# Performance work log

Hardware: AMD Instinct MI355X
Metric: run time of the kernel (lower is better)

Reference implementation:

```python
import jax, jax.numpy as jnp
import numpy as np

B, S, E, H = 2, 2048, 1024, 16
D = E // H  # head_dim = 64

def setup_inputs() -> dict:
    key = jax.random.key(0)
    k1, k2, k3 = jax.random.split(key, 3)
    x = jax.random.normal(k1, (B, S, E), dtype=jnp.float32)
    W_attn = jax.random.normal(k2, (E, 3 * E), dtype=jnp.float32) * 0.02
    b_attn = jnp.zeros((3 * E,), dtype=jnp.float32)
    W_proj = jax.random.normal(k3, (E, E), dtype=jnp.float32) * 0.02
    b_proj = jnp.zeros((E,), dtype=jnp.float32)
    return {"x": x, "W_attn": W_attn, "b_attn": b_attn, "W_proj": W_proj, "b_proj": b_proj}

def reference(x, W_attn, b_attn, W_proj, b_proj):
    bsz, seq, emb = x.shape
    # fused QKV projection (Conv1D == linear with [in,out] weight)
    qkv = x @ W_attn + b_attn                       # [B,S,3E]
    q, k, v = jnp.split(qkv, 3, axis=-1)
    def to_heads(t):
        return t.reshape(bsz, seq, H, D).transpose(0, 2, 1, 3)  # [B,H,S,D]
    q, k, v = to_heads(q), to_heads(k), to_heads(v)
    scale = jnp.float32(D) ** -0.5
    scores = jnp.einsum('bhqd,bhkd->bhqk', q, k) * scale        # [B,H,S,S]
    causal = jnp.tril(jnp.ones((seq, seq), dtype=bool))
    scores = jnp.where(causal, scores, jnp.float32(-jnp.inf))
    attn = jax.nn.softmax(scores, axis=-1)
    out = jnp.einsum('bhqk,bhkd->bhqd', attn, v)                # [B,H,S,D]
    out = out.transpose(0, 2, 1, 3).reshape(bsz, seq, emb)
    y = out @ W_proj + b_proj
    return y
```

## Files before the change

kernel.cpp:

```cpp
#include <hip/hip_runtime.h>
#include <hip/hip_bf16.h>


typedef __bf16 bf16;
typedef __bf16 bf16x4 __attribute__((ext_vector_type(4)));
typedef __bf16 bf16x8 __attribute__((ext_vector_type(8)));
typedef float  f32x4  __attribute__((ext_vector_type(4)));

#define MNEG (-1.0e30f)
#define QSCALE 0.1803368801f

__device__ __forceinline__ void gload16(const bf16* g, bf16* l) {
  __builtin_amdgcn_global_load_lds((const __attribute__((address_space(1))) void*)g,
                                   (__attribute__((address_space(3))) void*)l, 16, 0, 0);
}

__global__ __launch_bounds__(256) void prep_k(const float* __restrict__ x, bf16* __restrict__ xb,
                                              const float* __restrict__ Wa, bf16* __restrict__ WaT,
                                              const float* __restrict__ Wp, bf16* __restrict__ WpT) {
  const int bid = blockIdx.x;
  if (bid < 2048) {
    const int i = bid * 256 + threadIdx.x;
    f32x4 a = ((const f32x4*)x)[2 * i], b = ((const f32x4*)x)[2 * i + 1];
    bf16x8 o;
    for (int j = 0; j < 4; ++j) { o[j] = (bf16)a[j]; o[4 + j] = (bf16)b[j]; }
    ((bf16x8*)xb)[i] = o;
    return;
  }
  __shared__ bf16 t[64][68];
  const float* in; bf16* out; int C, cx, cy;
  if (bid < 2816) { in = Wa; out = WaT; C = 3072; const int tt = bid - 2048; cx = tt % 48; cy = tt / 48; }
  else            { in = Wp; out = WpT; C = 1024; const int tt = bid - 2816; cx = tt % 16; cy = tt / 16; }
  const int R = 1024;
  const int c0 = cx * 64, r0 = cy * 64;
  const int lr = threadIdx.x >> 4;
  const int lc = (threadIdx.x & 15) * 4;
  for (int i = 0; i < 4; ++i) {
    int r = lr + i * 16;
    f32x4 v = *(const f32x4*)(in + (size_t)(r0 + r) * C + c0 + lc);
    bf16x4 b;
    for (int j = 0; j < 4; ++j) b[j] = (bf16)v[j];
    *(bf16x4*)&t[r][lc] = b;
  }
  __syncthreads();
  for (int i = 0; i < 4; ++i) {
    int c = lr + i * 16;
    bf16x4 v;
    for (int j = 0; j < 4; ++j) v[j] = t[lc + j][c];
    *(bf16x4*)(out + (size_t)(c0 + c) * R + r0 + lc) = v;
  }
}

template <int MODE, int BN>
__global__ __launch_bounds__(256) void gemm_bt(const bf16* __restrict__ A,
                                               const bf16* __restrict__ Bt,
                                               const float* __restrict__ bias,
                                               float* __restrict__ C,
                                               bf16* __restrict__ Qo,
                                               bf16* __restrict__ Ko,
                                               bf16* __restrict__ Vo,
                                               int M, int N, int K) {
  constexpr int NT = BN / 32;
  __shared__ bf16 As0[128 * 32], As1[128 * 32];
  __shared__ bf16 Bs0[BN * 32],  Bs1[BN * 32];
  const int tid = threadIdx.x;
  const int w = tid >> 6, l = tid & 63;
  const int nx = gridDim.x;
  const int nwg = nx * gridDim.y;
  const int flat = blockIdx.y * nx + blockIdx.x;
  const int swz = (flat & 7) * (nwg >> 3) + (flat >> 3);
  const int m0 = (swz / nx) * 128, n0 = (swz % nx) * BN;
  const int wm = w >> 1, wn = w & 1;
  const int fr = l & 15, fg = l >> 4;
  const int srow = l >> 2;
  const int scol = (l & 3) * 8;

  f32x4 acc[4][NT] = {};

  for (int k0 = 0; k0 < K; k0 += 64) {
    __syncthreads();
    for (int c = 0; c < 2; ++c) {
      const int rowA = 32 * w + 16 * c + srow;
      gload16(A + (size_t)(m0 + rowA) * K + k0 + scol,      As0 + (32 * w + 16 * c) * 32);
      gload16(A + (size_t)(m0 + rowA) * K + k0 + 32 + scol, As1 + (32 * w + 16 * c) * 32);
    }
    for (int c = 0; c < BN / 64; ++c) {
      const int rb = (BN / 64) * 16 * w + 16 * c;
      gload16(Bt + (size_t)(n0 + rb + srow) * K + k0 + scol,      Bs0 + rb * 32);
      gload16(Bt + (size_t)(n0 + rb + srow) * K + k0 + 32 + scol, Bs1 + rb * 32);
    }
    __syncthreads();

    bf16x8 af[4][2], bfv[NT][2];
    for (int mt = 0; mt < 4; ++mt) {
      af[mt][0] = *(const bf16x8*)(As0 + (wm * 64 + mt * 16 + fr) * 32 + 8 * fg);
      af[mt][1] = *(const bf16x8*)(As1 + (wm * 64 + mt * 16 + fr) * 32 + 8 * fg);
    }
    for (int nt = 0; nt < NT; ++nt) {
      bfv[nt][0] = *(const bf16x8*)(Bs0 + (wn * (BN / 2) + nt * 16 + fr) * 32 + 8 * fg);
      bfv[nt][1] = *(const bf16x8*)(Bs1 + (wn * (BN / 2) + nt * 16 + fr) * 32 + 8 * fg);
    }
    for (int mt = 0; mt < 4; ++mt)
      for (int nt = 0; nt < NT; ++nt) {
        acc[mt][nt] = __builtin_amdgcn_mfma_f32_16x16x32_bf16(af[mt][0], bfv[nt][0], acc[mt][nt], 0, 0, 0);
        acc[mt][nt] = __builtin_amdgcn_mfma_f32_16x16x32_bf16(af[mt][1], bfv[nt][1], acc[mt][nt], 0, 0, 0);
      }
  }

  for (int mt = 0; mt < 4; ++mt) {
    for (int nt = 0; nt < NT; ++nt) {
      const int row0 = m0 + wm * 64 + mt * 16 + 4 * fg;
      const int col = n0 + wn * (BN / 2) + nt * 16 + fr;
      const float bv = bias[col];
      if (MODE == 0) {
        for (int r = 0; r < 4; ++r)
          C[(size_t)(row0 + r) * N + col] = acc[mt][nt][r] + bv;
      } else {
        const int which = col >> 10, h = (col >> 6) & 15, d = col & 63;
        const int b = row0 >> 11, s = row0 & 2047;
        if (which == 2) {
          bf16x4 vv;
          for (int r = 0; r < 4; ++r) vv[r] = (bf16)(acc[mt][nt][r] + bv);
          *(bf16x4*)(Vo + ((size_t)(b * 16 + h) * 64 + d) * 2048 + s) = vv;
        } else if (which == 0) {
          for (int r = 0; r < 4; ++r)
            Qo[((size_t)(b * 16 + h) * 2048 + s + r) * 64 + d] =
                (bf16)((acc[mt][nt][r] + bv) * QSCALE);
        } else {
          for (int r = 0; r < 4; ++r)
            Ko[((size_t)(b * 16 + h) * 2048 + s + r) * 64 + d] = (bf16)(acc[mt][nt][r] + bv);
        }
      }
    }
  }
}

__global__ __launch_bounds__(256, 3) void attn_k(const bf16* __restrict__ Qw,
                                                 const bf16* __restrict__ Kw,
                                                 const bf16* __restrict__ VtG,
                                                 bf16* __restrict__ AO) {
  __shared__ bf16 Ks[128 * 72];
  __shared__ bf16 Vt[64 * 136];
  __shared__ bf16 Ps[4 * 16 * 72];
  const int tid = threadIdx.x, w = tid >> 6, l = tid & 63;
  const int bid = blockIdx.x;
  const int bh = ((bid & 7) << 2) | ((bid >> 3) & 3);
  const int qt = 31 - (bid >> 5);
  const int q0 = qt * 64;
  const int fr = l & 15, fg = l >> 4;
  const size_t base = (size_t)bh * 2048 * 64;
  const int qw0 = q0 + w * 16;
  const int q = qw0 + fr;
  bf16* Pw = Ps + w * 16 * 72;
  const int r8 = tid >> 3, c8 = (tid & 7) * 8;
  const int r16 = tid >> 4, c16 = (tid & 15) * 8;

  bf16x8 qf[2];
  for (int t = 0; t < 2; ++t)
    qf[t] = *(const bf16x8*)(Qw + base + (size_t)(qw0 + fr) * 64 + 32 * t + 8 * fg);

  f32x4 oacc[4] = {};
  float lsum = 0.f;
  bf16x8 kreg[4], vreg[4];

  auto load_tile = [&](int kt) {
    for (int c = 0; c < 4; ++c) {
      kreg[c] = *(const bf16x8*)(Kw + base + (size_t)(kt + r8 + 32 * c) * 64 + c8);
      vreg[c] = *(const bf16x8*)(VtG + base + (size_t)(r16 + 16 * c) * 2048 + kt + c16);
    }
  };
  auto write_tile = [&]() {
    for (int c = 0; c < 4; ++c) {
      *(bf16x8*)(Ks + (r8 + 32 * c) * 72 + c8) = kreg[c];
      *(bf16x8*)(Vt + (r16 + 16 * c) * 136 + c16) = vreg[c];
    }
  };

  load_tile(0);
  write_tile();
  __syncthreads();

  for (int kt = 0; kt <= q0; kt += 128) {
    const bool havenext = (kt + 128 <= q0);
    if (havenext) load_tile(kt + 128);

    for (int h = 0; h < 2; ++h) {
      const int kh = kt + 64 * h;
      if (kh > q0) break;

      f32x4 sc[4];
      __builtin_amdgcn_s_setprio(1);
      for (int c = 0; c < 4; ++c) {
        bf16x8 kf0 = *(const bf16x8*)(Ks + (64 * h + c * 16 + fr) * 72 + 8 * fg);
        bf16x8 kf1 = *(const bf16x8*)(Ks + (64 * h + c * 16 + fr) * 72 + 32 + 8 * fg);
        f32x4 z = {};
        z = __builtin_amdgcn_mfma_f32_16x16x32_bf16(kf0, qf[0], z, 0, 0, 0);
        sc[c] = __builtin_amdgcn_mfma_f32_16x16x32_bf16(kf1, qf[1], z, 0, 0, 0);
      }
      __builtin_amdgcn_s_setprio(0);

      const bool need_mask = (kh + 63 > qw0);
      float psum = 0.f;
      for (int c = 0; c < 4; ++c) {
        bf16x4 pb;
        for (int r = 0; r < 4; ++r) {
          float s = sc[c][r];
          if (need_mask && (kh + c * 16 + 4 * fg + r > q)) s = MNEG;
          const float pv = __builtin_amdgcn_exp2f(s);
          psum += pv;
          pb[r] = (bf16)pv;
        }
        *(bf16x4*)(Pw + fr * 72 + c * 16 + 4 * fg) = pb;
      }
      psum += __shfl_xor(psum, 16, 64);
      psum += __shfl_xor(psum, 32, 64);
      lsum += psum;

      asm volatile("" ::: "memory");
      __builtin_amdgcn_s_setprio(1);
      for (int t = 0; t < 2; ++t) {
        bf16x8 pa = *(const bf16x8*)(Pw + fr * 72 + 32 * t + 8 * fg);
        for (int dt = 0; dt < 4; ++dt) {
          bf16x8 vf = *(const bf16x8*)(Vt + (dt * 16 + fr) * 136 + 64 * h + 32 * t + 8 * fg);
          oacc[dt] = __builtin_amdgcn_mfma_f32_16x16x32_bf16(pa, vf, oacc[dt], 0, 0, 0);
        }
      }
      __builtin_amdgcn_s_setprio(0);
      asm volatile("" ::: "memory");
    }

    if (!havenext) break;
    __syncthreads();
    write_tile();
    __syncthreads();
  }

  const int b = bh >> 4, h = bh & 15;
  float linv[4];
  for (int r = 0; r < 4; ++r)
    linv[r] = 1.f / __shfl(lsum, (l & 48) | (4 * fg + r), 64);
  for (int dt = 0; dt < 4; ++dt)
    for (int r = 0; r < 4; ++r) {
      const int qq = qw0 + 4 * fg + r;
      AO[(size_t)(b * 2048 + qq) * 1024 + h * 64 + dt * 16 + fr] =
          (bf16)(oacc[dt][r] * linv[r]);
    }
}

extern "C" void kernel_launch(void* const* d_in, const int* in_sizes, int n_in,
                              void* d_out, int out_size, void* d_ws, size_t ws_size,
                              hipStream_t stream) {
  const float* x      = (const float*)d_in[0];
  const float* W_attn = (const float*)d_in[1];
  const float* b_attn = (const float*)d_in[2];
  const float* W_proj = (const float*)d_in[3];
  const float* b_proj = (const float*)d_in[4];
  float* out = (float*)d_out;

  char* ws = (char*)d_ws;
  bf16* WaT = (bf16*)(ws);
  bf16* WpT = (bf16*)(ws + 6291456);
  bf16* Qw  = (bf16*)(ws + 8388608);
  bf16* Kw  = (bf16*)(ws + 16777216);
  bf16* VtG = (bf16*)(ws + 25165824);
  bf16* AO  = (bf16*)(ws + 33554432);
  bf16* xb  = AO;

  prep_k<<<3072, 256, 0, stream>>>(x, xb, W_attn, WaT, W_proj, WpT);

  gemm_bt<1, 128><<<dim3(24, 32), 256, 0, stream>>>(
      xb, WaT, b_attn, nullptr, Qw, Kw, VtG, 4096, 3072, 1024);

  attn_k<<<1024, 256, 0, stream>>>(Qw, Kw, VtG, AO);

  gemm_bt<0, 64><<<dim3(16, 32), 256, 0, stream>>>(
      AO, WpT, b_proj, out, nullptr, nullptr, nullptr, 4096, 1024, 1024);
}
```

Baseline: 109.5 us.

## Split heavy causal attention tiles over KV range and merge in normalization kernel

The heaviest query tiles (the upper half of the sequence) are split into two blocks, each covering half of the KV range. Each writes unnormalized fp32 partial outputs and row sums to workspace. A new norm_k kernel adds the two partials, divides by the combined sum and writes bf16 output. This balances work across the grid and shortens the critical-path block, at the cost of an extra launch plus fp32 partial traffic. It works without a running max because scores are bounded and use a fixed offset. The split path runs only when the workspace is large enough.

```diff
diff --git a/kernel.cpp b/kernel.cpp
--- a/kernel.cpp
+++ b/kernel.cpp
@@ -135,18 +135,43 @@
   }
 }
 
+template <int SPLIT>
 __global__ __launch_bounds__(256, 3) void attn_k(const bf16* __restrict__ Qw,
                                                  const bf16* __restrict__ Kw,
                                                  const bf16* __restrict__ VtG,
-                                                 bf16* __restrict__ AO) {
+                                                 bf16* __restrict__ AO,
+                                                 float* __restrict__ Op,
+                                                 float* __restrict__ Lp) {
   __shared__ bf16 Ks[128 * 72];
   __shared__ bf16 Vt[64 * 136];
   __shared__ bf16 Ps[4 * 16 * 72];
   const int tid = threadIdx.x, w = tid >> 6, l = tid & 63;
   const int bid = blockIdx.x;
-  const int bh = ((bid & 7) << 2) | ((bid >> 3) & 3);
-  const int qt = 31 - (bid >> 5);
+
+  int bh, qt, part; bool heavy;
+  if (SPLIT && bid < 1024) {
+    bh = ((bid & 7) << 2) | ((bid >> 3) & 3);
+    const int rem = bid >> 5;
+    qt = 31 - (rem >> 1);
+    part = rem & 1;
+    heavy = true;
+  } else {
+    const int r = SPLIT ? bid - 1024 : bid;
+    bh = ((r & 7) << 2) | ((r >> 3) & 3);
+    qt = (SPLIT ? 15 : 31) - (r >> 5);
+    part = 0;
+    heavy = false;
+  }
+
   const int q0 = qt * 64;
+  const int nt = (qt >> 1) + 1;
+  int ktbeg = 0, ktend = q0;
+  if (heavy) {
+    const int lo = (nt + 1) >> 1;
+    if (part == 0) { ktbeg = 0;        ktend = (lo - 1) * 128; }
+    else           { ktbeg = lo * 128; ktend = (nt - 1) * 128; }
+  }
+
   const int fr = l & 15, fg = l >> 4;
   const size_t base = (size_t)bh * 2048 * 64;
   const int qw0 = q0 + w * 16;
@@ -176,12 +201,12 @@
     }
   };
 
-  load_tile(0);
+  load_tile(ktbeg);
   write_tile();
   __syncthreads();
 
-  for (int kt = 0; kt <= q0; kt += 128) {
-    const bool havenext = (kt + 128 <= q0);
+  for (int kt = ktbeg; kt <= ktend; kt += 128) {
+    const bool havenext = (kt + 128 <= ktend);
     if (havenext) load_tile(kt + 128);
 
     for (int h = 0; h < 2; ++h) {
@@ -235,16 +260,48 @@
     __syncthreads();
   }
 
-  const int b = bh >> 4, h = bh & 15;
-  float linv[4];
-  for (int r = 0; r < 4; ++r)
-    linv[r] = 1.f / __shfl(lsum, (l & 48) | (4 * fg + r), 64);
-  for (int dt = 0; dt < 4; ++dt)
-    for (int r = 0; r < 4; ++r) {
-      const int qq = qw0 + 4 * fg + r;
-      AO[(size_t)(b * 2048 + qq) * 1024 + h * 64 + dt * 16 + fr] =
-          (bf16)(oacc[dt][r] * linv[r]);
-    }
+  if (heavy) {
+    const size_t pb = ((size_t)part * 32 + bh) * 1024;
+    const int sl0 = qw0 - 1024;
+    for (int dt = 0; dt < 4; ++dt)
+      for (int r = 0; r < 4; ++r)
+        Op[(pb + sl0 + 4 * fg + r) * 64 + dt * 16 + fr] = oacc[dt][r];
+    if (fg == 0) Lp[pb + sl0 + fr] = lsum;
+  } else {
+    const int b = bh >> 4, h = bh & 15;
+    float linv[4];
+    for (int r = 0; r < 4; ++r)
+      linv[r] = 1.f / __shfl(lsum, (l & 48) | (4 * fg + r), 64);
+    for (int dt = 0; dt < 4; ++dt)
+      for (int r = 0; r < 4; ++r) {
+        const int qq = qw0 + 4 * fg + r;
+        AO[(size_t)(b * 2048 + qq) * 1024 + h * 64 + dt * 16 + fr] =
+            (bf16)(oacc[dt][r] * linv[r]);
+      }
+  }
+}
+
+__global__ __launch_bounds__(256) void norm_k(const float* __restrict__ Op,
+                                              const float* __restrict__ Lp,
+                                              bf16* __restrict__ AO) {
+  const int i = blockIdx.x * 256 + threadIdx.x;
+  const int d0 = (i & 7) * 8;
+  const int sl = (i >> 3) & 1023;
+  const int h  = (i >> 13) & 15;
+  const int b  = i >> 17;
+  const size_t bhs = ((size_t)(b * 16 + h)) * 1024 + sl;
+  const size_t PSTR = (size_t)32 * 1024;
+  const float linv = 1.f / (Lp[bhs] + Lp[PSTR + bhs]);
+  const float* o0 = Op + bhs * 64 + d0;
+  const float* o1 = Op + PSTR * 64 + bhs * 64 + d0;
+  f32x4 a0 = *(const f32x4*)o0, a1 = *(const f32x4*)(o0 + 4);
+  f32x4 b0 = *(const f32x4*)o1, b1 = *(const f32x4*)(o1 + 4);
+  bf16x8 o;
+  for (int j = 0; j < 4; ++j) {
+    o[j]     = (bf16)((a0[j] + b0[j]) * linv);
+    o[4 + j] = (bf16)((a1[j] + b1[j]) * linv);
+  }
+  *(bf16x8*)(AO + ((size_t)(b * 2048) + 1024 + sl) * 1024 + h * 64 + d0) = o;
 }
 
 extern "C" void kernel_launch(void* const* d_in, const int* in_sizes, int n_in,
@@ -265,13 +322,21 @@
   bf16* VtG = (bf16*)(ws + 25165824);
   bf16* AO  = (bf16*)(ws + 33554432);
   bf16* xb  = AO;
+  float* Op = (float*)(ws + 41943040);
+  float* Lp = (float*)(ws + 58720256);
+  const bool split = (ws_size >= (size_t)58982400);
 
   prep_k<<<3072, 256, 0, stream>>>(x, xb, W_attn, WaT, W_proj, WpT);
 
   gemm_bt<1, 128><<<dim3(24, 32), 256, 0, stream>>>(
       xb, WaT, b_attn, nullptr, Qw, Kw, VtG, 4096, 3072, 1024);
 
-  attn_k<<<1024, 256, 0, stream>>>(Qw, Kw, VtG, AO);
+  if (split) {
+    attn_k<1><<<1536, 256, 0, stream>>>(Qw, Kw, VtG, AO, Op, Lp);
+    norm_k<<<1024, 256, 0, stream>>>(Op, Lp, AO);
+  } else {
+    attn_k<0><<<1024, 256, 0, stream>>>(Qw, Kw, VtG, AO, nullptr, nullptr);
+  }
 
   gemm_bt<0, 64><<<dim3(16, 32), 256, 0, stream>>>(
       AO, WpT, b_proj, out, nullptr, nullptr, nullptr, 4096, 1024, 1024);
```

Result: slower. 116.0 us (+5.9%).
